# Kernel optimization log

Measured on AMD Instinct MI355X. Metric: run time of the kernel, lower is better.

The kernel has to match this reference:

```python
import jax, jax.numpy as jnp
import numpy as np

O, I, B, G, BITS = 11008, 4096, 2048, 128, 3
N = I // G  # n_groups = 32
# Lloyd-Max optimal 8-level quantizer for unit Gaussian (3-bit PolarQuant codebook)
LLOYD_MAX_3BIT = [-2.1519, -1.3439, -0.7560, -0.2451, 0.2451, 0.7560, 1.3439, 2.1519]


def fwht(v):
    """Unnormalized fast Walsh-Hadamard transform along last axis (power-of-2 length)."""
    g = v.shape[-1]
    y = v.reshape(-1, g)
    h = 1
    while h < g:
        y = y.reshape(-1, g // (2 * h), 2, h)
        a, b = y[:, :, 0, :], y[:, :, 1, :]
        y = jnp.stack([a + b, a - b], axis=2).reshape(-1, g)
        h *= 2
    return y.reshape(v.shape)


def rotate(v, s1, s2):
    """Orthonormal randomized rotation R(v) = D2 * H * D1 * v / sqrt(G)."""
    g = v.shape[-1]
    return s2 * fwht(v * s1) * (1.0 / jnp.sqrt(jnp.asarray(g, v.dtype)))


def unpack3(packed):
    """Unpack 3-bit indices: [..., G//8*3] uint8 -> [..., G] int32 (matches unpack_indices)."""
    p = packed.reshape(*packed.shape[:-1], -1, 3).astype(jnp.int32)
    b0, b1, b2 = p[..., 0], p[..., 1], p[..., 2]
    outs = [
        b0 & 7, (b0 >> 3) & 7, ((b0 >> 6) | (b1 << 2)) & 7, (b1 >> 1) & 7,
        (b1 >> 4) & 7, ((b1 >> 7) | (b2 << 1)) & 7, (b2 >> 2) & 7, (b2 >> 5) & 7,
    ]
    return jnp.stack(outs, axis=-1).reshape(*packed.shape[:-1], -1)


def setup_inputs() -> dict:
    key = jax.random.key(0)
    kx, kw, k1, k2 = jax.random.split(key, 4)
    centroids = jnp.asarray(LLOYD_MAX_3BIT, dtype=jnp.float32)
    signs1 = jnp.where(jax.random.bernoulli(k1, 0.5, (G,)), 1.0, -1.0).astype(jnp.float32)
    signs2 = jnp.where(jax.random.bernoulli(k2, 0.5, (G,)), 1.0, -1.0).astype(jnp.float32)
    x = jax.random.normal(kx, (B, I), dtype=jnp.float32)
    # Quantize a dense weight exactly as TurboQuantWrapper.__init__ does.
    W = jax.random.normal(kw, (O, I), dtype=jnp.float32) * 0.02
    grouped = W.reshape(O, N, G)
    r = rotate(grouped, signs1, signs2)                     # [O,N,G] rotated groups
    gnorm = jnp.sqrt((r * r).sum(-1))                        # [O,N] (= ||w|| per group)
    dirn = r * jnp.sqrt(jnp.float32(G)) / (gnorm[..., None] + 1e-12)
    bnd = (centroids[:-1] + centroids[1:]) * 0.5
    idx = jnp.searchsorted(bnd, dirn)                        # nearest-centroid [O,N,G]
    q = centroids[idx]
    # norm correction: least-squares rescale of group norm against codebook hits
    norms = gnorm * (dirn * q).sum(-1) / ((q * q).sum(-1) + 1e-12)   # [O,N]
    # 3-bit packing: 8 indices -> 3 bytes (pack_indices, bits=3)
    v = np.asarray(idx, dtype=np.int32).reshape(O * N, G // 8, 8)
    b0 = v[..., 0] | (v[..., 1] << 3) | ((v[..., 2] & 3) << 6)
    b1 = (v[..., 2] >> 2) | (v[..., 3] << 1) | (v[..., 4] << 4) | ((v[..., 5] & 1) << 7)
    b2 = (v[..., 5] >> 1) | (v[..., 6] << 2) | (v[..., 7] << 5)
    packed = np.stack([b0, b1, b2], axis=-1).astype(np.uint8).reshape(O * N, G // 8 * 3)
    return {
        "x": x,
        "packed_weight": jnp.asarray(packed),
        "norms": norms.astype(jnp.float32),
        "centroids": centroids,
        "signs1": signs1,
        "signs2": signs2,
    }


def reference(x, packed_weight, norms, centroids, signs1, signs2):
    o, n = norms.shape
    g = signs1.shape[0]
    idx = unpack3(packed_weight.reshape(o, n, -1))           # [O,N,G] int32
    # FWHT-on-input: rotate each input group (fused kernel's input transform)
    rx = rotate(x.reshape(x.shape[0], n, g), signs1, signs2)  # [B,N,G]
    # Dequantized weight in rotated space: norm * centroid / sqrt(G)
    wq = centroids[idx] * (norms / jnp.sqrt(jnp.float32(g)))[:, :, None]  # [O,N,G]
    # x . w = R(x) . R(w) since R is orthonormal
    return jnp.einsum("bng,ong->bo", rx, wq)                 # [B,O]
```

## Files before the change

kernel.cpp:

```cpp
#include <hip/hip_runtime.h>

typedef unsigned int u32;
typedef unsigned short u16;

typedef short bf16x8 __attribute__((ext_vector_type(8)));
typedef float f32x4 __attribute__((ext_vector_type(4)));

#define GM 2048
#define GN 11008
#define GK 4096
#define NGRP 32
#define GSZ 128

#define CAST_G(p) ((const __attribute__((address_space(1))) void*)(p))
#define CAST_L(p) ((__attribute__((address_space(3))) void*)(p))
#define BAR() __builtin_amdgcn_s_barrier()
#define SCHED0() __builtin_amdgcn_sched_barrier(0)

__device__ __forceinline__ u16 f2bf(float f) {
    u32 u = __builtin_bit_cast(u32, f);
    u32 r = (u + 0x7FFFu + ((u >> 16) & 1u)) >> 16;
    return (u16)r;
}

__device__ __forceinline__ float cent3(int i) {
    int m3 = (i >= 4) ? (i - 4) : (3 - i);
    float mag = (m3 >= 2) ? ((m3 == 3) ? 2.1519f : 1.3439f)
                          : ((m3 == 1) ? 0.756f  : 0.2451f);
    return (i >= 4) ? mag : -mag;
}

#define ROT_BLOCKS (GM * NGRP / 4)
#define DQ_BLOCKS  (GN * NGRP * 4 / 256)

__global__ __launch_bounds__(256) void prep_kernel(
    const float* __restrict__ x, const float* __restrict__ s1,
    const float* __restrict__ s2, u32* __restrict__ rx,
    const u32* __restrict__ p32, const float* __restrict__ norms,
    u16* __restrict__ wq) {
    if (blockIdx.x < ROT_BLOCKS) {
        int gid  = blockIdx.x * 256 + threadIdx.x;
        int grp  = gid >> 6;
        int lane = gid & 63;

        const float2* xp = (const float2*)(x + (size_t)grp * GSZ);
        float2 xv  = xp[lane];
        float2 s1v = ((const float2*)s1)[lane];
        float2 s2v = ((const float2*)s2)[lane];

        float e0 = xv.x * s1v.x;
        float e1 = xv.y * s1v.y;
        {
            float a = e0 + e1, b = e0 - e1;
            e0 = a; e1 = b;
        }
        #pragma unroll
        for (int hb = 1; hb <= 32; hb <<= 1) {
            float t0 = __shfl_xor(e0, hb, 64);
            float t1 = __shfl_xor(e1, hb, 64);
            bool up = (lane & hb) != 0;
            e0 = up ? (t0 - e0) : (e0 + t0);
            e1 = up ? (t1 - e1) : (e1 + t1);
        }
        const float inv = 0.08838834764831845f;
        u32 lo = f2bf(e0 * s2v.x * inv);
        u32 hi = f2bf(e1 * s2v.y * inv);
        rx[gid] = lo | (hi << 16);
    } else {
        int u = (blockIdx.x - ROT_BLOCKS) * 256 + threadIdx.x;
        int g_idx = u >> 2;

        float scale = norms[g_idx] * 0.08838834764831845f;

        u32 w0 = p32[(size_t)u * 3 + 0];
        u32 w1 = p32[(size_t)u * 3 + 1];
        u32 w2 = p32[(size_t)u * 3 + 2];

        u32 tri[4];
        if (((w0 | w1 | w2) & 0xFFFFFF00u) == 0u) {
            const u32* pi = p32 + (size_t)u * 12;
            u32 b[12];
            #pragma unroll
            for (int k = 0; k < 12; ++k) b[k] = pi[k];
            #pragma unroll
            for (int t = 0; t < 4; ++t)
                tri[t] = b[3*t] | (b[3*t+1] << 8) | (b[3*t+2] << 16);
        } else {
            tri[0] = w0 & 0xFFFFFFu;
            tri[1] = (w0 >> 24) | ((w1 & 0xFFFFu) << 8);
            tri[2] = (w1 >> 16) | ((w2 & 0xFFu) << 16);
            tri[3] = w2 >> 8;
        }

        u32 ow[16];
        #pragma unroll
        for (int t = 0; t < 4; ++t) {
            u32 v = tri[t];
            #pragma unroll
            for (int k = 0; k < 4; ++k) {
                int i0 = (int)((v >> (6*k))     & 7u);
                int i1 = (int)((v >> (6*k + 3)) & 7u);
                u32 lo = f2bf(cent3(i0) * scale);
                u32 hi = f2bf(cent3(i1) * scale);
                ow[t*4 + k] = lo | (hi << 16);
            }
        }
        u32* op = (u32*)(wq + (size_t)u * 32);
        #pragma unroll
        for (int k = 0; k < 16; ++k) op[k] = ow[k];
    }
}

__device__ __forceinline__ void stage_half(const u16* g, char* ldst, int rowOff, int tt) {
    __builtin_amdgcn_global_load_lds(CAST_G(g + (size_t)rowOff * GK + tt * 64),
                                     CAST_L(ldst), 16, 0, 0);
    __builtin_amdgcn_global_load_lds(CAST_G(g + (size_t)(rowOff + 64) * GK + tt * 64),
                                     CAST_L(ldst + 8192), 16, 0, 0);
}

template<int BUF>
__device__ __forceinline__ void ktile4(int t, char* lds,
                                       const u16* gA, const u16* gB,
                                       int sB, int aBase, int bBase, int sw0, int sw1,
                                       f32x4 (&acc)[8][4]) {
    const int AB  = BUF * 32768;
    const int ABo = (BUF ^ 1) * 32768;
    const int BB  = 65536 + BUF * 32768;

    bf16x8 aF[4][2], b0F[2][2], b1F[2][2];
    bool s1 = (t < 63), s2 = (t < 62);

    #pragma unroll
    for (int mj = 0; mj < 4; ++mj) {
        aF[mj][0] = *(const bf16x8*)(lds + AB + aBase + mj * 4096 + sw0);
        aF[mj][1] = *(const bf16x8*)(lds + AB + aBase + mj * 4096 + sw1);
    }
    #pragma unroll
    for (int nj = 0; nj < 2; ++nj) {
        b0F[nj][0] = *(const bf16x8*)(lds + BB + bBase + nj * 8192 + sw0);
        b0F[nj][1] = *(const bf16x8*)(lds + BB + bBase + nj * 8192 + sw1);
    }
    #pragma unroll
    for (int nj = 0; nj < 2; ++nj) {
        b1F[nj][0] = *(const bf16x8*)(lds + BB + 16384 + bBase + nj * 8192 + sw0);
        b1F[nj][1] = *(const bf16x8*)(lds + BB + 16384 + bBase + nj * 8192 + sw1);
    }
    SCHED0();
    __builtin_amdgcn_s_setprio(1);
    #pragma unroll
    for (int kk = 0; kk < 2; ++kk) {
        #pragma unroll
        for (int mj = 0; mj < 4; ++mj)
            #pragma unroll
            for (int nj = 0; nj < 2; ++nj)
                acc[mj][nj] = __builtin_amdgcn_mfma_f32_16x16x32_bf16(
                    aF[mj][kk], b0F[nj][kk], acc[mj][nj], 0, 0, 0);
        #pragma unroll
        for (int mj = 0; mj < 4; ++mj)
            #pragma unroll
            for (int nj = 0; nj < 2; ++nj)
                acc[mj][2 + nj] = __builtin_amdgcn_mfma_f32_16x16x32_bf16(
                    aF[mj][kk], b1F[nj][kk], acc[mj][2 + nj], 0, 0, 0);
    }
    __builtin_amdgcn_s_setprio(0);
    if (s1) stage_half(gA, lds + ABo + 16384 + sB, 128, t + 1);
    BAR();

    #pragma unroll
    for (int mj = 0; mj < 4; ++mj) {
        aF[mj][0] = *(const bf16x8*)(lds + AB + 16384 + aBase + mj * 4096 + sw0);
        aF[mj][1] = *(const bf16x8*)(lds + AB + 16384 + aBase + mj * 4096 + sw1);
    }
    SCHED0();
    __builtin_amdgcn_s_setprio(1);
    #pragma unroll
    for (int kk = 0; kk < 2; ++kk) {
        #pragma unroll
        for (int mj = 0; mj < 4; ++mj)
            #pragma unroll
            for (int nj = 0; nj < 2; ++nj)
                acc[4 + mj][nj] = __builtin_amdgcn_mfma_f32_16x16x32_bf16(
                    aF[mj][kk], b0F[nj][kk], acc[4 + mj][nj], 0, 0, 0);
        #pragma unroll
        for (int mj = 0; mj < 4; ++mj)
            #pragma unroll
            for (int nj = 0; nj < 2; ++nj)
                acc[4 + mj][2 + nj] = __builtin_amdgcn_mfma_f32_16x16x32_bf16(
                    aF[mj][kk], b1F[nj][kk], acc[4 + mj][2 + nj], 0, 0, 0);
    }
    __builtin_amdgcn_s_setprio(0);
    if (s2) {
        stage_half(gA, lds + AB + sB,         0,   t + 2);
        stage_half(gB, lds + BB + sB,         0,   t + 2);
        stage_half(gB, lds + BB + 16384 + sB, 128, t + 2);
    }
    if (s2) { asm volatile("s_waitcnt vmcnt(6)" ::: "memory"); }
    else    { asm volatile("s_waitcnt vmcnt(0)" ::: "memory"); }
    BAR();
}

__device__ __forceinline__ void gemm_big(int tau, int tid, char* lds,
                                         const u16* A, const u16* Bw, float* C) {
    int lane = tid & 63;
    int wv   = tid >> 6;
    int wr   = wv >> 2;
    int wc   = wv & 3;

    int n0 = (tau & 31) * 256;
    int m0 = (tau >> 5) * 256;

    int srow = tid >> 3;
    int c16  = (tid & 7) ^ (srow & 7);
    const u16* gA = A  + (size_t)(m0 + srow) * GK + c16 * 8;
    const u16* gB = Bw + (size_t)(n0 + srow) * GK + c16 * 8;
    int sB = wv * 1024;

    int aBase = (wr * 16 + (lane & 15)) * 128;
    int bBase = (wc * 16 + (lane & 15)) * 128;
    int sw0 = (((lane >> 4))     ^ (lane & 7)) << 4;
    int sw1 = (((lane >> 4) + 4) ^ (lane & 7)) << 4;

    f32x4 acc[8][4] = {};

    stage_half(gA, lds + sB,                 0,   0);
    stage_half(gB, lds + 65536 + sB,         0,   0);
    stage_half(gA, lds + 16384 + sB,         128, 0);
    stage_half(gB, lds + 65536 + 16384 + sB, 128, 0);
    stage_half(gA, lds + 32768 + sB,         0,   1);
    stage_half(gB, lds + 65536 + 32768 + sB, 0,   1);
    stage_half(gB, lds + 98304 + 16384 + sB, 128, 1);
    asm volatile("s_waitcnt vmcnt(6)" ::: "memory");
    BAR();

    for (int tt = 0; tt < 64; tt += 2) {
        ktile4<0>(tt,     lds, gA, gB, sB, aBase, bBase, sw0, sw1, acc);
        ktile4<1>(tt + 1, lds, gA, gB, sB, aBase, bBase, sw0, sw1, acc);
    }

    int cr = (lane >> 4) * 4;
    int cc = lane & 15;
    #pragma unroll
    for (int mh = 0; mh < 2; ++mh)
        #pragma unroll
        for (int mj = 0; mj < 4; ++mj)
            #pragma unroll
            for (int nh = 0; nh < 2; ++nh)
                #pragma unroll
                for (int nj = 0; nj < 2; ++nj) {
                    float* cp = C + (size_t)(m0 + mh * 128 + wr * 16 + mj * 32 + cr) * GN
                                  + (n0 + nh * 128 + wc * 16 + nj * 64 + cc);
                    #pragma unroll
                    for (int j = 0; j < 4; ++j)
                        __builtin_nontemporal_store(acc[mh * 4 + mj][nh * 2 + nj][j],
                                                    cp + (size_t)j * GN);
                }
}

template<int BUF>
__device__ __forceinline__ void ktile2(int t, char* lds,
                                       const u16* gA, const u16* gB,
                                       int sB, int aBase, int bBase, int sw0, int sw1,
                                       f32x4 (&acc)[4][4]) {
    const int AB  = BUF * 16384;
    const int BB  = 49152 + BUF * 32768;
    const int NB  = (BUF + 2 >= 3) ? (BUF - 1) : (BUF + 2);
    const int ABn = NB * 16384;
    const int BBn = 49152 + NB * 32768;

    bf16x8 aF[4][2], bF[2][2];
    bool s2 = (t < 62);

    #pragma unroll
    for (int mj = 0; mj < 4; ++mj) {
        aF[mj][0] = *(const bf16x8*)(lds + AB + aBase + mj * 4096 + sw0);
        aF[mj][1] = *(const bf16x8*)(lds + AB + aBase + mj * 4096 + sw1);
    }
    #pragma unroll
    for (int nj = 0; nj < 2; ++nj) {
        bF[nj][0] = *(const bf16x8*)(lds + BB + bBase + nj * 8192 + sw0);
        bF[nj][1] = *(const bf16x8*)(lds + BB + bBase + nj * 8192 + sw1);
    }
    SCHED0();
    __builtin_amdgcn_s_setprio(1);
    #pragma unroll
    for (int kk = 0; kk < 2; ++kk)
        #pragma unroll
        for (int mj = 0; mj < 4; ++mj)
            #pragma unroll
            for (int nj = 0; nj < 2; ++nj)
                acc[mj][nj] = __builtin_amdgcn_mfma_f32_16x16x32_bf16(
                    aF[mj][kk], bF[nj][kk], acc[mj][nj], 0, 0, 0);
    __builtin_amdgcn_s_setprio(0);
    if (s2) {
        stage_half(gA, lds + ABn + sB, 0, t + 2);
        stage_half(gB, lds + BBn + sB, 0, t + 2);
    }
    BAR();

    #pragma unroll
    for (int nj = 0; nj < 2; ++nj) {
        bF[nj][0] = *(const bf16x8*)(lds + BB + 16384 + bBase + nj * 8192 + sw0);
        bF[nj][1] = *(const bf16x8*)(lds + BB + 16384 + bBase + nj * 8192 + sw1);
    }
    SCHED0();
    __builtin_amdgcn_s_setprio(1);
    #pragma unroll
    for (int kk = 0; kk < 2; ++kk)
        #pragma unroll
        for (int mj = 0; mj < 4; ++mj)
            #pragma unroll
            for (int nj = 0; nj < 2; ++nj)
                acc[mj][2 + nj] = __builtin_amdgcn_mfma_f32_16x16x32_bf16(
                    aF[mj][kk], bF[nj][kk], acc[mj][2 + nj], 0, 0, 0);
    __builtin_amdgcn_s_setprio(0);
    if (s2) stage_half(gB, lds + BBn + 16384 + sB, 128, t + 2);
    if (s2) { asm volatile("s_waitcnt vmcnt(6)" ::: "memory"); }
    else    { asm volatile("s_waitcnt vmcnt(0)" ::: "memory"); }
    BAR();
}

__device__ __forceinline__ void gemm_tail(int bid, int tid, char* lds,
                                          const u16* A, const u16* Bw, float* C) {
    int lane = tid & 63;
    int wv   = tid >> 6;
    int wr   = wv >> 2;
    int wc   = wv & 3;

    int x = bid & 7, s = bid >> 3;
    int nt, mh;
    if (s < 16) { nt = x; mh = s; }
    else { int idx = (s - 16) * 8 + x; nt = 8 + (idx >> 4); mh = idx & 15; }
    int m0  = mh * 128;
    int n0  = 8192 + nt * 256;

    int srow = tid >> 3;
    int c16  = (tid & 7) ^ (srow & 7);
    const u16* gA = A  + (size_t)(m0 + srow) * GK + c16 * 8;
    const u16* gB = Bw + (size_t)(n0 + srow) * GK + c16 * 8;
    int sB = wv * 1024;

    int aBase = (wr * 16 + (lane & 15)) * 128;
    int bBase = (wc * 16 + (lane & 15)) * 128;
    int sw0 = (((lane >> 4))     ^ (lane & 7)) << 4;
    int sw1 = (((lane >> 4) + 4) ^ (lane & 7)) << 4;

    f32x4 acc[4][4] = {};

    stage_half(gA, lds + sB,                 0,   0);
    stage_half(gB, lds + 49152 + sB,         0,   0);
    stage_half(gB, lds + 49152 + 16384 + sB, 128, 0);
    stage_half(gA, lds + 16384 + sB,         0,   1);
    stage_half(gB, lds + 81920 + sB,         0,   1);
    stage_half(gB, lds + 81920 + 16384 + sB, 128, 1);
    asm volatile("s_waitcnt vmcnt(6)" ::: "memory");
    BAR();

    for (int tt = 0; tt < 63; tt += 3) {
        ktile2<0>(tt,     lds, gA, gB, sB, aBase, bBase, sw0, sw1, acc);
        ktile2<1>(tt + 1, lds, gA, gB, sB, aBase, bBase, sw0, sw1, acc);
        ktile2<2>(tt + 2, lds, gA, gB, sB, aBase, bBase, sw0, sw1, acc);
    }
    ktile2<0>(63, lds, gA, gB, sB, aBase, bBase, sw0, sw1, acc);

    int cr = (lane >> 4) * 4;
    int cc = lane & 15;
    #pragma unroll
    for (int mj = 0; mj < 4; ++mj)
        #pragma unroll
        for (int nj = 0; nj < 4; ++nj) {
            float* cp = C + (size_t)(m0 + wr * 16 + mj * 32 + cr) * GN
                          + (n0 + wc * 16 + nj * 64 + cc);
            #pragma unroll
            for (int j = 0; j < 4; ++j)
                __builtin_nontemporal_store(acc[mj][nj][j], cp + (size_t)j * GN);
        }
}

__global__ __launch_bounds__(512, 1) void gemm_all_kernel(
    const u16* __restrict__ A, const u16* __restrict__ Bw,
    float* __restrict__ C) {
    extern __shared__ char lds[];
    int bid = blockIdx.x;
    if (bid < 256) gemm_big (bid,       threadIdx.x, lds, A, Bw, C);
    else           gemm_tail(bid - 256, threadIdx.x, lds, A, Bw, C);
}

extern "C" void kernel_launch(void* const* d_in, const int* in_sizes, int n_in,
                              void* d_out, int out_size, void* d_ws, size_t ws_size,
                              hipStream_t stream) {
    const float* x      = (const float*)d_in[0];
    const void*  packed = d_in[1];
    const float* norms  = (const float*)d_in[2];
    const float* s1     = (const float*)d_in[4];
    const float* s2     = (const float*)d_in[5];
    float* out          = (float*)d_out;

    size_t rx_bytes = (size_t)GM * GK * 2;
    size_t wq_bytes = (size_t)GN * GK * 2;
    if (ws_size < rx_bytes + wq_bytes) return;

    u16* rx = (u16*)d_ws;
    u16* wq = rx + (size_t)GM * GK;

    prep_kernel<<<dim3(ROT_BLOCKS + DQ_BLOCKS), dim3(256), 0, stream>>>(
        x, s1, s2, (u32*)rx, (const u32*)packed, norms, wq);

    hipFuncSetAttribute((const void*)gemm_all_kernel,
                        hipFuncAttributeMaxDynamicSharedMemorySize, 147456);
    gemm_all_kernel<<<dim3(432), dim3(512), 147456, stream>>>(rx, wq, out);
}
```

Measured before the change: 206.1 us.

## Triple-buffer A tiles in LDS to issue A prefetches earlier

Changes the LDS staging from double buffers for both A and B to three rotating A buffers plus two B buffers, with the main loop unrolled by six to cycle the buffer indices. A loads for tile t+2 can then be issued during the first half of tile t rather than after the second MFMA block, which gives global loads more time to land before they are consumed. LDS use grows to 160KB per block, and the loop body roughly triples in code size.

```diff
diff --git a/kernel.cpp b/kernel.cpp
--- a/kernel.cpp
+++ b/kernel.cpp
@@ -118,14 +118,15 @@
                                      CAST_L(ldst + 8192), 16, 0, 0);
 }
 
-template<int BUF>
+template<int AB_I, int BB_I>
 __device__ __forceinline__ void ktile4(int t, char* lds,
                                        const u16* gA, const u16* gB,
                                        int sB, int aBase, int bBase, int sw0, int sw1,
                                        f32x4 (&acc)[8][4]) {
-    const int AB  = BUF * 32768;
-    const int ABo = (BUF ^ 1) * 32768;
-    const int BB  = 65536 + BUF * 32768;
+    const int AB  = AB_I * 32768;
+    const int ABn = ((AB_I + 2) % 3) * 32768;
+    const int BB  = 98304 + BB_I * 32768;
+    const int BBo = 98304 + (BB_I ^ 1) * 32768;
 
     bf16x8 aF[4][2], b0F[2][2], b1F[2][2];
     bool s1 = (t < 63), s2 = (t < 62);
@@ -163,7 +164,8 @@
                     aF[mj][kk], b1F[nj][kk], acc[mj][2 + nj], 0, 0, 0);
     }
     __builtin_amdgcn_s_setprio(0);
-    if (s1) stage_half(gA, lds + ABo + 16384 + sB, 128, t + 1);
+    if (s1) stage_half(gB, lds + BBo + 16384 + sB, 128, t + 1);
+    if (s2) stage_half(gA, lds + ABn + sB,         0,   t + 2);
     BAR();
 
     #pragma unroll
@@ -190,9 +192,8 @@
     }
     __builtin_amdgcn_s_setprio(0);
     if (s2) {
-        stage_half(gA, lds + AB + sB,         0,   t + 2);
-        stage_half(gB, lds + BB + sB,         0,   t + 2);
-        stage_half(gB, lds + BB + 16384 + sB, 128, t + 2);
+        stage_half(gB, lds + BB + sB,          0,   t + 2);
+        stage_half(gA, lds + ABn + 16384 + sB, 128, t + 2);
     }
     if (s2) { asm volatile("s_waitcnt vmcnt(6)" ::: "memory"); }
     else    { asm volatile("s_waitcnt vmcnt(0)" ::: "memory"); }
@@ -222,20 +223,28 @@
 
     f32x4 acc[8][4] = {};
 
-    stage_half(gA, lds + sB,                 0,   0);
-    stage_half(gB, lds + 65536 + sB,         0,   0);
-    stage_half(gA, lds + 16384 + sB,         128, 0);
-    stage_half(gB, lds + 65536 + 16384 + sB, 128, 0);
-    stage_half(gA, lds + 32768 + sB,         0,   1);
-    stage_half(gB, lds + 65536 + 32768 + sB, 0,   1);
-    stage_half(gB, lds + 98304 + 16384 + sB, 128, 1);
+    stage_half(gA, lds + sB,                  0,   0);
+    stage_half(gA, lds + 16384 + sB,          128, 0);
+    stage_half(gB, lds + 98304 + sB,          0,   0);
+    stage_half(gB, lds + 98304 + 16384 + sB,  128, 0);
+    stage_half(gA, lds + 32768 + sB,          0,   1);
+    stage_half(gA, lds + 32768 + 16384 + sB,  128, 1);
+    stage_half(gB, lds + 131072 + sB,         0,   1);
     asm volatile("s_waitcnt vmcnt(6)" ::: "memory");
     BAR();
 
-    for (int tt = 0; tt < 64; tt += 2) {
-        ktile4<0>(tt,     lds, gA, gB, sB, aBase, bBase, sw0, sw1, acc);
-        ktile4<1>(tt + 1, lds, gA, gB, sB, aBase, bBase, sw0, sw1, acc);
-    }
+    for (int tt = 0; tt < 60; tt += 6) {
+        ktile4<0,0>(tt,     lds, gA, gB, sB, aBase, bBase, sw0, sw1, acc);
+        ktile4<1,1>(tt + 1, lds, gA, gB, sB, aBase, bBase, sw0, sw1, acc);
+        ktile4<2,0>(tt + 2, lds, gA, gB, sB, aBase, bBase, sw0, sw1, acc);
+        ktile4<0,1>(tt + 3, lds, gA, gB, sB, aBase, bBase, sw0, sw1, acc);
+        ktile4<1,0>(tt + 4, lds, gA, gB, sB, aBase, bBase, sw0, sw1, acc);
+        ktile4<2,1>(tt + 5, lds, gA, gB, sB, aBase, bBase, sw0, sw1, acc);
+    }
+    ktile4<0,0>(60, lds, gA, gB, sB, aBase, bBase, sw0, sw1, acc);
+    ktile4<1,1>(61, lds, gA, gB, sB, aBase, bBase, sw0, sw1, acc);
+    ktile4<2,0>(62, lds, gA, gB, sB, aBase, bBase, sw0, sw1, acc);
+    ktile4<0,1>(63, lds, gA, gB, sB, aBase, bBase, sw0, sw1, acc);
 
     int cr = (lane >> 4) * 4;
     int cc = lane & 15;
@@ -406,6 +415,6 @@
         x, s1, s2, (u32*)rx, (const u32*)packed, norms, wq);
 
     hipFuncSetAttribute((const void*)gemm_all_kernel,
-                        hipFuncAttributeMaxDynamicSharedMemorySize, 147456);
-    gemm_all_kernel<<<dim3(432), dim3(512), 147456, stream>>>(rx, wq, out);
-}
+                        hipFuncAttributeMaxDynamicSharedMemorySize, 163840);
+    gemm_all_kernel<<<dim3(432), dim3(512), 163840, stream>>>(rx, wq, out);
+}
```

Result: no change. 203.3 us, median of 3 (-1.4%).
